# Performance work log

Measured on AMD Instinct MI355X. Metric: run time of the kernel, lower is better.

The kernel has to match this reference:

```python
import jax, jax.numpy as jnp
import numpy as np

B, C, HW = 128, 3, 224
P = 16
D = 256
NH = 8
HD = D // NH
E = 4            # num_experts
K = 2            # top-k
FF = 4 * D
NC = 38
EPS = 1e-5


def _layernorm(x, g, b):
    mu = jnp.mean(x, axis=-1, keepdims=True)
    var = jnp.mean(jnp.square(x - mu), axis=-1, keepdims=True)
    return (x - mu) * jax.lax.rsqrt(var + EPS) * g + b


def setup_inputs() -> dict:
    key = jax.random.key(0)
    ks = jax.random.split(key, 16)
    s = 0.02
    return {
        "x": jax.random.normal(ks[0], (B, C, HW, HW), dtype=jnp.float32),
        "conv_w": jax.random.normal(ks[1], (D, C, P, P), dtype=jnp.float32) * s,
        "conv_b": jnp.zeros((D,), jnp.float32),
        "cls_token": jnp.zeros((1, 1, D), jnp.float32),
        "ln1_g": jnp.ones((D,), jnp.float32),
        "ln1_b": jnp.zeros((D,), jnp.float32),
        "qkv_w": jax.random.normal(ks[2], (3 * D, D), dtype=jnp.float32) * s,
        "qkv_b": jnp.zeros((3 * D,), jnp.float32),
        "out_w": jax.random.normal(ks[3], (D, D), dtype=jnp.float32) * s,
        "out_b": jnp.zeros((D,), jnp.float32),
        "ln2_g": jnp.ones((D,), jnp.float32),
        "ln2_b": jnp.zeros((D,), jnp.float32),
        "router_w": jax.random.normal(ks[4], (E, D), dtype=jnp.float32) * s,
        "router_b": jnp.zeros((E,), jnp.float32),
        "e_w1": jax.random.normal(ks[5], (E, D, FF), dtype=jnp.float32) * s,
        "e_b1": jnp.zeros((E, FF), jnp.float32),
        "e_w2": jax.random.normal(ks[6], (E, FF, D), dtype=jnp.float32) * s,
        "e_b2": jnp.zeros((E, D), jnp.float32),
        "head_w": jax.random.normal(ks[7], (NC, D), dtype=jnp.float32) * s,
        "head_b": jnp.zeros((NC,), jnp.float32),
    }


def reference(x, conv_w, conv_b, cls_token, ln1_g, ln1_b, qkv_w, qkv_b,
              out_w, out_b, ln2_g, ln2_b, router_w, router_b,
              e_w1, e_b1, e_w2, e_b2, head_w, head_b):
    # patch embed: Conv2d(3, D, 16, 16) -> [B, D, 14, 14] -> [B, 196, D]
    h = jax.lax.conv_general_dilated(
        x, conv_w, window_strides=(P, P), padding="VALID",
        dimension_numbers=("NCHW", "OIHW", "NCHW")) + conv_b[None, :, None, None]
    b = h.shape[0]
    tok = h.reshape(b, D, -1).transpose(0, 2, 1)            # [B, 196, D]
    tok = jnp.concatenate([jnp.broadcast_to(cls_token, (b, 1, D)), tok], axis=1)  # [B, 197, D]
    S = tok.shape[1]

    # Multi-head self-attention (pre-norm)
    x2 = _layernorm(tok, ln1_g, ln1_b)
    qkv = x2 @ qkv_w.T + qkv_b                              # [B, S, 3D]
    q, k, v = jnp.split(qkv, 3, axis=-1)
    q = q.reshape(b, S, NH, HD)
    k = k.reshape(b, S, NH, HD)
    v = v.reshape(b, S, NH, HD)
    scores = jnp.einsum("bqhd,bkhd->bhqk", q, k) / np.float32(np.sqrt(HD))
    attn = jax.nn.softmax(scores, axis=-1)
    ao = jnp.einsum("bhqk,bkhd->bqhd", attn, v).reshape(b, S, D)
    ao = ao @ out_w.T + out_b
    tok = tok + ao

    # MoE FFN (pre-norm). NOTE: original code computes top-k routing weights
    # but never multiplies outputs by them — outputs of selected experts are
    # simply summed. We reproduce that faithfully.
    x2 = _layernorm(tok, ln2_g, ln2_b)
    x_flat = x2.reshape(-1, D)                              # [T, D]
    logits = x_flat @ router_w.T + router_b                 # [T, E]
    probs = jax.nn.softmax(logits, axis=-1)
    _topw, topi = jax.lax.top_k(probs, K)                   # topw unused (as in source)
    mask = (topi[..., None] == jnp.arange(E)).any(axis=1)   # [T, E] bool
    out_flat = jnp.zeros_like(x_flat)
    for i in range(E):                                       # fixed small expert count
        hid = jax.nn.gelu(x_flat @ e_w1[i] + e_b1[i], approximate=False)
        out_flat = out_flat + mask[:, i:i + 1].astype(x_flat.dtype) * (hid @ e_w2[i] + e_b2[i])
    tok = tok + out_flat.reshape(b, S, D)

    return tok[:, 0] @ head_w.T + head_b                    # [B, NC]
```

## Files before the change

kernel.cpp:

```cpp
#include <hip/hip_runtime.h>
#include <hip/hip_bf16.h>
#include <math.h>

#define TTOK   25216
#define SEQL   197
#define NBATCH 128
#define DMODEL 256
#define NHEADS 8
#define FFD    1024
#define NEXP   4
#define NCLS   38
#define CONVK  768
#define NPATCH 196
#define CM     25088

typedef unsigned short u16;
typedef unsigned int u32;
using s16x8 = __attribute__((ext_vector_type(8))) short;
using f32x4 = __attribute__((ext_vector_type(4))) float;

__device__ __forceinline__ float b2f(u16 v) {
  union { unsigned u; float f; } x; x.u = (unsigned)v << 16; return x.f;
}
__device__ __forceinline__ u16 f2b(float f) {
  __hip_bfloat16 h = __float2bfloat16(f);
  return *reinterpret_cast<u16*>(&h);
}
__device__ __forceinline__ void gload16(const void* g, void* l) {
  __builtin_amdgcn_global_load_lds(
      (const __attribute__((address_space(1))) void*)g,
      (__attribute__((address_space(3))) void*)l, 16, 0, 0);
}
__device__ __forceinline__ float warp_sum(float v) {
  #pragma unroll
  for (int o = 32; o; o >>= 1) v += __shfl_xor(v, o);
  return v;
}
__device__ __forceinline__ float warp_max(float v) {
  #pragma unroll
  for (int o = 32; o; o >>= 1) v = fmaxf(v, __shfl_xor(v, o));
  return v;
}
__device__ __forceinline__ int fsw(int row) { return (row ^ (row >> 2)) & 3; }

__global__ __launch_bounds__(256) void k_cast2(const float* __restrict__ in,
                                               u16* __restrict__ hi,
                                               u16* __restrict__ lo) {
  int i = (blockIdx.x * 256 + threadIdx.x) * 4;
  float4 v = *(const float4*)&in[i];
  float vv[4] = {v.x, v.y, v.z, v.w};
  u16 h[4], l[4];
  #pragma unroll
  for (int j = 0; j < 4; ++j) {
    h[j] = f2b(vv[j]);
    l[j] = f2b(vv[j] - b2f(h[j]));
  }
  *(uint2*)&hi[i] = *(const uint2*)h;
  *(uint2*)&lo[i] = *(const uint2*)l;
}

__global__ __launch_bounds__(256) void k_conv(const float* __restrict__ x,
                                              const u16* __restrict__ cwh,
                                              const u16* __restrict__ cwl,
                                              const float* __restrict__ cb,
                                              float* __restrict__ tok) {
  const int n0 = blockIdx.x * 128;
  const int m0 = blockIdx.y * 64;
  __shared__ __align__(16) u16 lds[2 * 64 * 40 + 2 * 128 * 32];
  u16* Ah_s = lds;
  u16* Al_s = lds + 64 * 40;
  u16* Wh_s = lds + 2 * 64 * 40;
  u16* Wl_s = lds + 2 * 64 * 40 + 128 * 32;
  const int tid = threadIdx.x;
  const int lane = tid & 63;
  const int wv = tid >> 6;
  const int wr = wv >> 1, wc = wv & 1;
  const int l15 = lane & 15, l4 = lane >> 4;
  f32x4 acc[2][4] = {};

  const int kpos = (tid & 7) * 4;
  long abase[2]; int aldso[2];
  #pragma unroll
  for (int it = 0; it < 2; ++it) {
    int row = it * 32 + (tid >> 3);
    int m = m0 + row;
    int b = m / NPATCH, p = m - b * NPATCH;
    int py = p / 14, px = p - py * 14;
    abase[it] = (long)(b * 3) * 50176 + (py * 16) * 224 + px * 16;
    aldso[it] = row * 80 + kpos * 2;
  }
  long woff[2]; int wofs[2];
  #pragma unroll
  for (int r = 0; r < 2; ++r) {
    int off = r * 4096 + tid * 16;
    int row = off >> 6;
    int c16 = (off >> 4) & 3;
    int kk = (c16 ^ fsw(row)) << 3;
    woff[r] = (long)(n0 + row) * CONVK + kk;
    wofs[r] = off;
  }
  for (int kc = 0; kc < CONVK; kc += 32) {
    #pragma unroll
    for (int r = 0; r < 2; ++r) {
      gload16(cwh + woff[r] + kc, (char*)Wh_s + wofs[r]);
      gload16(cwl + woff[r] + kc, (char*)Wl_s + wofs[r]);
    }
    int k = kc + kpos;
    int c = k >> 8, r8 = k & 255;
    long soff = (long)c * 50176 + (r8 >> 4) * 224 + (r8 & 15);
    #pragma unroll
    for (int it = 0; it < 2; ++it) {
      float4 v = *(const float4*)&x[abase[it] + soff];
      float vv[4] = {v.x, v.y, v.z, v.w};
      u16 h[4], l[4];
      #pragma unroll
      for (int j = 0; j < 4; ++j) {
        h[j] = f2b(vv[j]);
        l[j] = f2b(vv[j] - b2f(h[j]));
      }
      *(uint2*)((char*)Ah_s + aldso[it]) = *(const uint2*)h;
      *(uint2*)((char*)Al_s + aldso[it]) = *(const uint2*)l;
    }
    __syncthreads();
    s16x8 ah[2], al[2], bh[4], bl[4];
    #pragma unroll
    for (int i = 0; i < 2; ++i) {
      int rowa = wr * 32 + i * 16 + l15;
      ah[i] = *(const s16x8*)((const char*)Ah_s + rowa * 80 + l4 * 16);
      al[i] = *(const s16x8*)((const char*)Al_s + rowa * 80 + l4 * 16);
    }
    #pragma unroll
    for (int j = 0; j < 4; ++j) {
      int rowb = wc * 64 + j * 16 + l15;
      int kbb = (l4 ^ fsw(rowb)) << 4;
      bh[j] = *(const s16x8*)((const char*)Wh_s + rowb * 64 + kbb);
      bl[j] = *(const s16x8*)((const char*)Wl_s + rowb * 64 + kbb);
    }
    #pragma unroll
    for (int i = 0; i < 2; ++i)
      #pragma unroll
      for (int j = 0; j < 4; ++j)
        acc[i][j] = __builtin_amdgcn_mfma_f32_16x16x32_bf16(ah[i], bh[j],
                                                            acc[i][j], 0, 0, 0);
    #pragma unroll
    for (int i = 0; i < 2; ++i)
      #pragma unroll
      for (int j = 0; j < 4; ++j)
        acc[i][j] = __builtin_amdgcn_mfma_f32_16x16x32_bf16(ah[i], bl[j],
                                                            acc[i][j], 0, 0, 0);
    #pragma unroll
    for (int i = 0; i < 2; ++i)
      #pragma unroll
      for (int j = 0; j < 4; ++j)
        acc[i][j] = __builtin_amdgcn_mfma_f32_16x16x32_bf16(al[i], bh[j],
                                                            acc[i][j], 0, 0, 0);
    __syncthreads();
  }
  const int mb = m0 + wr * 32 + (l4 << 2);
  const int nb = n0 + wc * 64 + l15;
  #pragma unroll
  for (int i = 0; i < 2; ++i) {
    #pragma unroll
    for (int jf = 0; jf < 4; ++jf) {
      #pragma unroll
      for (int j = 0; j < 4; ++j) {
        int m = mb + i * 16 + j;
        int n = nb + jf * 16;
        int bq = m / NPATCH;
        long cr = (long)bq * SEQL + (m - bq * NPATCH) + 1;
        tok[cr * DMODEL + n] = acc[i][jf][j] + cb[n];
      }
    }
  }
}

__global__ __launch_bounds__(256) void k_lnstat(const float* __restrict__ in,
                                                float2* __restrict__ st) {
  const int row = blockIdx.x * 4 + (threadIdx.x >> 6);
  const int lane = threadIdx.x & 63;
  float4 v = *(const float4*)&in[(size_t)row * DMODEL + lane * 4];
  float s1 = v.x + v.y + v.z + v.w;
  float s2 = v.x * v.x + v.y * v.y + v.z * v.z + v.w * v.w;
  s1 = warp_sum(s1);
  s2 = warp_sum(s2);
  if (lane == 0) {
    float mu = s1 * (1.f / DMODEL);
    float var = s2 * (1.f / DMODEL) - mu * mu;
    st[row] = make_float2(mu, rsqrtf(var + 1e-5f));
  }
}

__global__ __launch_bounds__(256) void k_qkv(const float* __restrict__ tok,
                                             const float2* __restrict__ stats,
                                             const float* __restrict__ g,
                                             const float* __restrict__ bb,
                                             const u16* __restrict__ Wh,
                                             const u16* __restrict__ Wl,
                                             const float* __restrict__ bias,
                                             float* __restrict__ Cf) {
  const int n0 = blockIdx.x * 128;
  const int m0 = blockIdx.y * 128;
  __shared__ __align__(16) u16 lds[2 * 128 * 40 + 2 * 128 * 32];
  u16* Ah_s = lds;
  u16* Al_s = lds + 128 * 40;
  u16* Wh_s = lds + 2 * 128 * 40;
  u16* Wl_s = lds + 2 * 128 * 40 + 128 * 32;
  const int tid = threadIdx.x;
  const int lane = tid & 63;
  const int wv = tid >> 6;
  const int wr = wv >> 1, wc = wv & 1;
  const int l15 = lane & 15, l4 = lane >> 4;
  f32x4 acc[4][4] = {};

  const int kpos = (tid & 7) * 4;
  long atok[4]; float2 st[4]; int aldso[4];
  #pragma unroll
  for (int it = 0; it < 4; ++it) {
    int row = it * 32 + (tid >> 3);
    int m = m0 + row;
    atok[it] = (long)m * DMODEL;
    st[it] = stats[m];
    aldso[it] = row * 80 + kpos * 2;
  }
  long woff[2]; int wofs[2];
  #pragma unroll
  for (int r = 0; r < 2; ++r) {
    int off = r * 4096 + tid * 16;
    int row = off >> 6;
    int c16 = (off >> 4) & 3;
    int kk = (c16 ^ fsw(row)) << 3;
    woff[r] = (long)(n0 + row) * DMODEL + kk;
    wofs[r] = off;
  }
  for (int kc = 0; kc < DMODEL; kc += 32) {
    #pragma unroll
    for (int r = 0; r < 2; ++r) {
      gload16(Wh + woff[r] + kc, (char*)Wh_s + wofs[r]);
      gload16(Wl + woff[r] + kc, (char*)Wl_s + wofs[r]);
    }
    float4 g4 = *(const float4*)&g[kc + kpos];
    float4 b4 = *(const float4*)&bb[kc + kpos];
    float gg[4] = {g4.x, g4.y, g4.z, g4.w};
    float bbv[4] = {b4.x, b4.y, b4.z, b4.w};
    #pragma unroll
    for (int it = 0; it < 4; ++it) {
      float4 v = *(const float4*)&tok[atok[it] + kc + kpos];
      float vv[4] = {v.x, v.y, v.z, v.w};
      u16 h[4], l[4];
      #pragma unroll
      for (int j = 0; j < 4; ++j) {
        float xd = (vv[j] - st[it].x) * st[it].y * gg[j] + bbv[j];
        h[j] = f2b(xd);
        l[j] = f2b(xd - b2f(h[j]));
      }
      *(uint2*)((char*)Ah_s + aldso[it]) = *(const uint2*)h;
      *(uint2*)((char*)Al_s + aldso[it]) = *(const uint2*)l;
    }
    __syncthreads();
    s16x8 ah[4], al[4], bh[4], bl[4];
    #pragma unroll
    for (int i = 0; i < 4; ++i) {
      int rowa = wr * 64 + i * 16 + l15;
      ah[i] = *(const s16x8*)((const char*)Ah_s + rowa * 80 + l4 * 16);
      al[i] = *(const s16x8*)((const char*)Al_s + rowa * 80 + l4 * 16);
      int rowb = wc * 64 + i * 16 + l15;
      int kbb = (l4 ^ fsw(rowb)) << 4;
      bh[i] = *(const s16x8*)((const char*)Wh_s + rowb * 64 + kbb);
      bl[i] = *(const s16x8*)((const char*)Wl_s + rowb * 64 + kbb);
    }
    #pragma unroll
    for (int i = 0; i < 4; ++i)
      #pragma unroll
      for (int j = 0; j < 4; ++j)
        acc[i][j] = __builtin_amdgcn_mfma_f32_16x16x32_bf16(ah[i], bh[j],
                                                            acc[i][j], 0, 0, 0);
    #pragma unroll
    for (int i = 0; i < 4; ++i)
      #pragma unroll
      for (int j = 0; j < 4; ++j)
        acc[i][j] = __builtin_amdgcn_mfma_f32_16x16x32_bf16(ah[i], bl[j],
                                                            acc[i][j], 0, 0, 0);
    #pragma unroll
    for (int i = 0; i < 4; ++i)
      #pragma unroll
      for (int j = 0; j < 4; ++j)
        acc[i][j] = __builtin_amdgcn_mfma_f32_16x16x32_bf16(al[i], bh[j],
                                                            acc[i][j], 0, 0, 0);
    __syncthreads();
  }
  const int mb = m0 + wr * 64 + (l4 << 2);
  const int nb = n0 + wc * 64 + l15;
  #pragma unroll
  for (int i = 0; i < 4; ++i) {
    #pragma unroll
    for (int jf = 0; jf < 4; ++jf) {
      #pragma unroll
      for (int j = 0; j < 4; ++j) {
        int m = mb + i * 16 + j;
        int n = nb + jf * 16;
        Cf[(long)m * 512 + n] = acc[i][jf][j] + bias[n];
      }
    }
  }
}

__global__ void k_cls(const float* __restrict__ cls, float* __restrict__ tok) {
  tok[(size_t)blockIdx.x * SEQL * DMODEL + threadIdx.x] = cls[threadIdx.x];
}

__global__ __launch_bounds__(256) void k_qcls(const float* __restrict__ tok,
                                              const float2* __restrict__ stats,
                                              const float* __restrict__ g,
                                              const float* __restrict__ bb,
                                              const u16* __restrict__ qwh,
                                              const u16* __restrict__ qwl,
                                              const float* __restrict__ qb,
                                              u16* __restrict__ qch,
                                              u16* __restrict__ qcl) {
  const int b = blockIdx.x, n = threadIdx.x;
  __shared__ float xs[DMODEL];
  float2 st = stats[b * SEQL];
  float v = tok[(size_t)b * SEQL * DMODEL + n];
  xs[n] = (v - st.x) * st.y * g[n] + bb[n];
  __syncthreads();
  float val = qb[n];
  #pragma unroll 4
  for (int i = 0; i < 32; ++i) {
    s16x8 wh = *(const s16x8*)(qwh + (size_t)n * DMODEL + i * 8);
    s16x8 wl = *(const s16x8*)(qwl + (size_t)n * DMODEL + i * 8);
    #pragma unroll
    for (int j = 0; j < 8; ++j)
      val = fmaf(b2f((u16)wh[j]) + b2f((u16)wl[j]), xs[i * 8 + j], val);
  }
  u16 h = f2b(val);
  qch[b * DMODEL + n] = h;
  qcl[b * DMODEL + n] = f2b(val - b2f(h));
}

__global__ __launch_bounds__(256) void k_attn_cls(const u16* __restrict__ qch,
                                                  const u16* __restrict__ qcl,
                                                  const float* __restrict__ kvf,
                                                  float* __restrict__ ao) {
  const int w = threadIdx.x >> 6, lane = threadIdx.x & 63;
  const int unit = blockIdx.x * 4 + w;
  const int b = unit >> 3, h = unit & 7;
  __shared__ float Ss[4][200];
  float q[32];
  #pragma unroll
  for (int i = 0; i < 4; ++i) {
    s16x8 vh = *(const s16x8*)(qch + b * DMODEL + h * 32 + i * 8);
    s16x8 vl = *(const s16x8*)(qcl + b * DMODEL + h * 32 + i * 8);
    #pragma unroll
    for (int j = 0; j < 8; ++j) q[i * 8 + j] = b2f((u16)vh[j]) + b2f((u16)vl[j]);
  }
  float sc[4];
  float mx = -1e30f;
  #pragma unroll
  for (int r = 0; r < 4; ++r) {
    int k = lane + 64 * r;
    float s = -1e30f;
    if (k < SEQL) {
      const float* kr = kvf + ((size_t)(b * SEQL + k)) * 512 + h * 32;
      s = 0.f;
      #pragma unroll
      for (int i = 0; i < 8; ++i) {
        float4 kv4 = *(const float4*)(kr + i * 4);
        s = fmaf(kv4.x, q[i * 4 + 0], s);
        s = fmaf(kv4.y, q[i * 4 + 1], s);
        s = fmaf(kv4.z, q[i * 4 + 2], s);
        s = fmaf(kv4.w, q[i * 4 + 3], s);
      }
      s *= 0.17677669529663687f;
    }
    sc[r] = s;
    mx = fmaxf(mx, s);
  }
  mx = warp_max(mx);
  float sm = 0.f;
  #pragma unroll
  for (int r = 0; r < 4; ++r) {
    int k = lane + 64 * r;
    float e = (k < SEQL) ? __expf(sc[r] - mx) : 0.f;
    sc[r] = e;
    sm += e;
  }
  sm = warp_sum(sm);
  float inv = 1.f / sm;
  #pragma unroll
  for (int r = 0; r < 4; ++r) {
    int k = lane + 64 * r;
    if (k < SEQL) Ss[w][k] = sc[r] * inv;
  }
  int d = lane & 31, half = lane >> 5;
  float acc = 0.f;
  for (int i = 0; i < 99; ++i) {
    int k = half * 99 + i;
    if (k < SEQL)
      acc = fmaf(Ss[w][k], kvf[((size_t)(b * SEQL + k)) * 512 + 256 + h * 32 + d], acc);
  }
  acc += __shfl_xor(acc, 32);
  if (lane < 32) ao[(b * NHEADS + h) * 32 + d] = acc;
}

__global__ __launch_bounds__(256) void k_oproj_route(
    const float* __restrict__ ao, const float* __restrict__ ow,
    const float* __restrict__ ob, const float* __restrict__ tok,
    const float* __restrict__ g, const float* __restrict__ bb,
    const float* __restrict__ rw, const float* __restrict__ rb,
    float* __restrict__ tokc, float* __restrict__ x2cf,
    float* __restrict__ maskf) {
  const int b = blockIdx.x, n = threadIdx.x;
  const int w = n >> 6, lane = n & 63;
  __shared__ float xs[DMODEL];
  __shared__ float xd_s[DMODEL];
  __shared__ float red[8];
  __shared__ float lg[4];
  xs[n] = ao[b * DMODEL + n];
  __syncthreads();
  float val = ob[n];
  #pragma unroll 4
  for (int i = 0; i < 64; ++i) {
    float4 wv = *(const float4*)(ow + (size_t)n * DMODEL + i * 4);
    val = fmaf(wv.x, xs[i * 4 + 0], val);
    val = fmaf(wv.y, xs[i * 4 + 1], val);
    val = fmaf(wv.z, xs[i * 4 + 2], val);
    val = fmaf(wv.w, xs[i * 4 + 3], val);
  }
  float t = tok[(size_t)b * SEQL * DMODEL + n] + val;
  tokc[b * DMODEL + n] = t;
  float s1 = warp_sum(t), s2 = warp_sum(t * t);
  if (lane == 0) { red[w] = s1; red[4 + w] = s2; }
  __syncthreads();
  s1 = red[0] + red[1] + red[2] + red[3];
  s2 = red[4] + red[5] + red[6] + red[7];
  float mu = s1 * (1.f / DMODEL);
  float var = s2 * (1.f / DMODEL) - mu * mu;
  float rs = rsqrtf(var + 1e-5f);
  float xd = (t - mu) * rs * g[n] + bb[n];
  x2cf[b * DMODEL + n] = xd;
  xd_s[n] = xd;
  __syncthreads();
  float s = 0.f;
  #pragma unroll
  for (int i = 0; i < 4; ++i) s = fmaf(xd_s[lane + i * 64], rw[w * DMODEL + lane + i * 64], s);
  s = warp_sum(s) + rb[w];
  if (lane == 0) lg[w] = s;
  __syncthreads();
  if (n < NEXP) {
    int e = n;
    int rank = 0;
    #pragma unroll
    for (int j = 0; j < NEXP; ++j)
      if (j != e && (lg[j] > lg[e] || (lg[j] == lg[e] && j < e))) ++rank;
    maskf[b * NEXP + e] = (rank < 2) ? 1.f : 0.f;
  }
}

__global__ __launch_bounds__(256) void k_moe1(const float* __restrict__ x2cf,
                                              const float* __restrict__ w1,
                                              const float* __restrict__ b1,
                                              const float* __restrict__ maskf,
                                              float* __restrict__ hid) {
  const int e = blockIdx.x, t = blockIdx.y;
  if (maskf[t * NEXP + e] == 0.f) return;
  __shared__ float xs[DMODEL];
  const int tid = threadIdx.x;
  xs[tid] = x2cf[t * DMODEL + tid];
  __syncthreads();
  const float* w1e = w1 + (size_t)e * DMODEL * FFD + tid;
  float a0 = 0.f, a1 = 0.f, a2 = 0.f, a3 = 0.f;
  #pragma unroll 4
  for (int k = 0; k < DMODEL; ++k) {
    float xv = xs[k];
    const float* wr_ = w1e + (size_t)k * FFD;
    a0 = fmaf(xv, wr_[0], a0);
    a1 = fmaf(xv, wr_[256], a1);
    a2 = fmaf(xv, wr_[512], a2);
    a3 = fmaf(xv, wr_[768], a3);
  }
  float accs[4] = {a0, a1, a2, a3};
  float* hrow = hid + ((size_t)e * NBATCH + t) * FFD;
  #pragma unroll
  for (int j = 0; j < 4; ++j) {
    float v = accs[j] + b1[e * FFD + tid + j * 256];
    hrow[tid + j * 256] = 0.5f * v * (1.0f + erff(v * 0.70710678118654752f));
  }
}

__global__ __launch_bounds__(256) void k_moe2(const float* __restrict__ hid,
                                              const float* __restrict__ w2,
                                              const float* __restrict__ b2,
                                              const float* __restrict__ maskf,
                                              float* __restrict__ tokc) {
  const int t = blockIdx.x, dc = blockIdx.y;
  const int tid = threadIdx.x;
  const int dl = tid & 127, kh = tid >> 7;
  const int dout = dc * 128 + dl;
  int e0 = 0;
  while (e0 < 3 && maskf[t * NEXP + e0] == 0.f) ++e0;
  int e1 = e0 + 1;
  while (e1 < 3 && maskf[t * NEXP + e1] == 0.f) ++e1;
  __shared__ float hs0[FFD], hs1[FFD];
  const float* h0 = hid + ((size_t)e0 * NBATCH + t) * FFD;
  const float* h1 = hid + ((size_t)e1 * NBATCH + t) * FFD;
  for (int i = tid * 4; i < FFD; i += 1024) {
    *(float4*)&hs0[i] = *(const float4*)&h0[i];
    *(float4*)&hs1[i] = *(const float4*)&h1[i];
  }
  __syncthreads();
  const float* w20 = w2 + (size_t)e0 * FFD * DMODEL + dout;
  const float* w21 = w2 + (size_t)e1 * FFD * DMODEL + dout;
  float a0 = 0.f, a1 = 0.f;
  const int k0 = kh * 512;
  #pragma unroll 8
  for (int k = k0; k < k0 + 512; ++k) {
    a0 = fmaf(hs0[k], w20[(size_t)k * DMODEL], a0);
    a1 = fmaf(hs1[k], w21[(size_t)k * DMODEL], a1);
  }
  __shared__ float red[256];
  red[tid] = a0 + a1;
  __syncthreads();
  if (kh == 0) {
    float full = red[dl] + red[128 + dl] +
                 b2[e0 * DMODEL + dout] + b2[e1 * DMODEL + dout];
    tokc[t * DMODEL + dout] += full;
  }
}

__global__ __launch_bounds__(256) void k_head(const float* __restrict__ tokc,
                                              const float* __restrict__ hw,
                                              const float* __restrict__ hb,
                                              float* __restrict__ out) {
  int b = blockIdx.x;
  int w = threadIdx.x >> 6, lane = threadIdx.x & 63;
  const float* row = tokc + (size_t)b * DMODEL;
  for (int c = w; c < NCLS; c += 4) {
    float s = 0.f;
    for (int d = lane; d < DMODEL; d += 64) s = fmaf(row[d], hw[c * DMODEL + d], s);
    s = warp_sum(s);
    if (lane == 0) out[b * NCLS + c] = s + hb[c];
  }
}

extern "C" void kernel_launch(void* const* d_in, const int* in_sizes, int n_in,
                              void* d_out, int out_size, void* d_ws, size_t ws_size,
                              hipStream_t stream) {
  const float* x      = (const float*)d_in[0];
  const float* conv_w = (const float*)d_in[1];
  const float* conv_b = (const float*)d_in[2];
  const float* cls    = (const float*)d_in[3];
  const float* ln1g   = (const float*)d_in[4];
  const float* ln1b   = (const float*)d_in[5];
  const float* qkv_w  = (const float*)d_in[6];
  const float* qkv_b  = (const float*)d_in[7];
  const float* out_w  = (const float*)d_in[8];
  const float* out_b  = (const float*)d_in[9];
  const float* ln2g   = (const float*)d_in[10];
  const float* ln2b   = (const float*)d_in[11];
  const float* rw     = (const float*)d_in[12];
  const float* rb     = (const float*)d_in[13];
  const float* e_w1   = (const float*)d_in[14];
  const float* e_b1   = (const float*)d_in[15];
  const float* e_w2   = (const float*)d_in[16];
  const float* e_b2   = (const float*)d_in[17];
  const float* head_w = (const float*)d_in[18];
  const float* head_b = (const float*)d_in[19];
  float* out = (float*)d_out;

  char* ws = (char*)d_ws;
  size_t off = 0;
  auto alloc = [&](size_t bytes) {
    void* p = ws + off;
    off += (bytes + 255) & ~(size_t)255;
    return p;
  };
  float*  tok   = (float*)alloc((size_t)TTOK * DMODEL * 4);
  float*  qkvf  = (float*)alloc((size_t)TTOK * 512 * 4);
  float2* stats = (float2*)alloc((size_t)TTOK * 8);
  u16*    cwh   = (u16*)alloc((size_t)DMODEL * CONVK * 2);
  u16*    cwl   = (u16*)alloc((size_t)DMODEL * CONVK * 2);
  u16*    qwh   = (u16*)alloc((size_t)768 * DMODEL * 2);
  u16*    qwl   = (u16*)alloc((size_t)768 * DMODEL * 2);
  u16*    qch   = (u16*)alloc((size_t)NBATCH * DMODEL * 2);
  u16*    qcl   = (u16*)alloc((size_t)NBATCH * DMODEL * 2);
  float*  aocf  = (float*)alloc((size_t)NBATCH * DMODEL * 4);
  float*  tokc  = (float*)alloc((size_t)NBATCH * DMODEL * 4);
  float*  x2cf  = (float*)alloc((size_t)NBATCH * DMODEL * 4);
  float*  maskf = (float*)alloc((size_t)NBATCH * NEXP * 4);
  float*  hid   = (float*)alloc((size_t)NEXP * NBATCH * FFD * 4);

  k_cast2<<<192, 256, 0, stream>>>(conv_w, cwh, cwl);
  k_cast2<<<192, 256, 0, stream>>>(qkv_w, qwh, qwl);

  k_conv<<<dim3(2, CM / 64), 256, 0, stream>>>(x, cwh, cwl, conv_b, tok);
  k_cls<<<NBATCH, DMODEL, 0, stream>>>(cls, tok);

  k_lnstat<<<TTOK / 4, 256, 0, stream>>>(tok, stats);

  k_qkv<<<dim3(4, TTOK / 128), 256, 0, stream>>>(
      tok, stats, ln1g, ln1b, qwh + 256 * DMODEL, qwl + 256 * DMODEL,
      qkv_b + 256, qkvf);

  k_qcls<<<NBATCH, 256, 0, stream>>>(tok, stats, ln1g, ln1b, qwh, qwl, qkv_b,
                                     qch, qcl);

  k_attn_cls<<<NBATCH * NHEADS / 4, 256, 0, stream>>>(qch, qcl, qkvf, aocf);

  k_oproj_route<<<NBATCH, 256, 0, stream>>>(aocf, out_w, out_b, tok,
                                            ln2g, ln2b, rw, rb,
                                            tokc, x2cf, maskf);

  k_moe1<<<dim3(NEXP, NBATCH), 256, 0, stream>>>(x2cf, e_w1, e_b1, maskf, hid);
  k_moe2<<<dim3(NBATCH, 2), 256, 0, stream>>>(hid, e_w2, e_b2, maskf, tokc);

  k_head<<<NBATCH, 256, 0, stream>>>(tokc, head_w, head_b, out);
}
```

Measured before the change: 212.9 us.

## Double-buffer weights and prefetch activations in conv and QKV GEMMs, enlarge conv tile

The conv and QKV GEMM kernels now double-buffer the weight tiles in LDS and prefetch the next K-chunk of activations into registers while the current chunk's MFMAs run, so global loads overlap with compute. The conv tile grows from 64 to 128 rows per block, giving more reuse per weight load and fewer blocks. The A-tile LDS row stride shrinks from 80 to 72 bytes, which requires split 8-byte reads, to change the bank pattern. The trade-off is higher register and LDS use per block, which may lower occupancy.

```diff
diff --git a/kernel.cpp b/kernel.cpp
--- a/kernel.cpp
+++ b/kernel.cpp
@@ -16,6 +16,7 @@
 
 typedef unsigned short u16;
 typedef unsigned int u32;
+using s16x4 = __attribute__((ext_vector_type(4))) short;
 using s16x8 = __attribute__((ext_vector_type(8))) short;
 using f32x4 = __attribute__((ext_vector_type(4))) float;
 
@@ -42,6 +43,12 @@
   return v;
 }
 __device__ __forceinline__ int fsw(int row) { return (row ^ (row >> 2)) & 3; }
+__device__ __forceinline__ s16x8 ldA72(const u16* base, int rowa, int l4) {
+  const char* p = (const char*)base + rowa * 72 + l4 * 16;
+  s16x4 a = *(const s16x4*)p;
+  s16x4 b = *(const s16x4*)(p + 8);
+  return __builtin_shufflevector(a, b, 0, 1, 2, 3, 4, 5, 6, 7);
+}
 
 __global__ __launch_bounds__(256) void k_cast2(const float* __restrict__ in,
                                                u16* __restrict__ hi,
@@ -65,29 +72,28 @@
                                               const float* __restrict__ cb,
                                               float* __restrict__ tok) {
   const int n0 = blockIdx.x * 128;
-  const int m0 = blockIdx.y * 64;
-  __shared__ __align__(16) u16 lds[2 * 64 * 40 + 2 * 128 * 32];
+  const int m0 = blockIdx.y * 128;
+  __shared__ __align__(16) u16 lds[25600];
   u16* Ah_s = lds;
-  u16* Al_s = lds + 64 * 40;
-  u16* Wh_s = lds + 2 * 64 * 40;
-  u16* Wl_s = lds + 2 * 64 * 40 + 128 * 32;
+  u16* Al_s = lds + 4608;
+  u16* Wbuf = lds + 9216;
   const int tid = threadIdx.x;
   const int lane = tid & 63;
   const int wv = tid >> 6;
   const int wr = wv >> 1, wc = wv & 1;
   const int l15 = lane & 15, l4 = lane >> 4;
-  f32x4 acc[2][4] = {};
+  f32x4 acc[4][4] = {};
 
   const int kpos = (tid & 7) * 4;
-  long abase[2]; int aldso[2];
-  #pragma unroll
-  for (int it = 0; it < 2; ++it) {
+  long abase[4]; int aldso[4];
+  #pragma unroll
+  for (int it = 0; it < 4; ++it) {
     int row = it * 32 + (tid >> 3);
     int m = m0 + row;
     int b = m / NPATCH, p = m - b * NPATCH;
     int py = p / 14, px = p - py * 14;
     abase[it] = (long)(b * 3) * 50176 + (py * 16) * 224 + px * 16;
-    aldso[it] = row * 80 + kpos * 2;
+    aldso[it] = row * 72 + kpos * 2;
   }
   long woff[2]; int wofs[2];
   #pragma unroll
@@ -99,19 +105,23 @@
     woff[r] = (long)(n0 + row) * CONVK + kk;
     wofs[r] = off;
   }
+  #pragma unroll
+  for (int r = 0; r < 2; ++r) {
+    gload16(cwh + woff[r], (char*)Wbuf + wofs[r]);
+    gload16(cwl + woff[r], (char*)Wbuf + 8192 + wofs[r]);
+  }
+  float4 xr[4];
+  {
+    int c = kpos >> 8, r8 = kpos & 255;
+    long soff = (long)c * 50176 + (r8 >> 4) * 224 + (r8 & 15);
+    #pragma unroll
+    for (int it = 0; it < 4; ++it) xr[it] = *(const float4*)&x[abase[it] + soff];
+  }
+  int cur = 0;
   for (int kc = 0; kc < CONVK; kc += 32) {
     #pragma unroll
-    for (int r = 0; r < 2; ++r) {
-      gload16(cwh + woff[r] + kc, (char*)Wh_s + wofs[r]);
-      gload16(cwl + woff[r] + kc, (char*)Wl_s + wofs[r]);
-    }
-    int k = kc + kpos;
-    int c = k >> 8, r8 = k & 255;
-    long soff = (long)c * 50176 + (r8 >> 4) * 224 + (r8 & 15);
-    #pragma unroll
-    for (int it = 0; it < 2; ++it) {
-      float4 v = *(const float4*)&x[abase[it] + soff];
-      float vv[4] = {v.x, v.y, v.z, v.w};
+    for (int it = 0; it < 4; ++it) {
+      float vv[4] = {xr[it].x, xr[it].y, xr[it].z, xr[it].w};
       u16 h[4], l[4];
       #pragma unroll
       for (int j = 0; j < 4; ++j) {
@@ -122,44 +132,56 @@
       *(uint2*)((char*)Al_s + aldso[it]) = *(const uint2*)l;
     }
     __syncthreads();
-    s16x8 ah[2], al[2], bh[4], bl[4];
-    #pragma unroll
-    for (int i = 0; i < 2; ++i) {
-      int rowa = wr * 32 + i * 16 + l15;
-      ah[i] = *(const s16x8*)((const char*)Ah_s + rowa * 80 + l4 * 16);
-      al[i] = *(const s16x8*)((const char*)Al_s + rowa * 80 + l4 * 16);
-    }
-    #pragma unroll
-    for (int j = 0; j < 4; ++j) {
-      int rowb = wc * 64 + j * 16 + l15;
+    if (kc + 32 < CONVK) {
+      char* wdst = (char*)Wbuf + ((cur ^ 1) << 14);
+      #pragma unroll
+      for (int r = 0; r < 2; ++r) {
+        gload16(cwh + woff[r] + kc + 32, wdst + wofs[r]);
+        gload16(cwl + woff[r] + kc + 32, wdst + 8192 + wofs[r]);
+      }
+      int k = kc + 32 + kpos;
+      int c = k >> 8, r8 = k & 255;
+      long soff = (long)c * 50176 + (r8 >> 4) * 224 + (r8 & 15);
+      #pragma unroll
+      for (int it = 0; it < 4; ++it) xr[it] = *(const float4*)&x[abase[it] + soff];
+    }
+    const char* Wcur = (const char*)Wbuf + (cur << 14);
+    s16x8 ah[4], al[4], bh[4], bl[4];
+    #pragma unroll
+    for (int i = 0; i < 4; ++i) {
+      int rowa = wr * 64 + i * 16 + l15;
+      ah[i] = ldA72(Ah_s, rowa, l4);
+      al[i] = ldA72(Al_s, rowa, l4);
+      int rowb = wc * 64 + i * 16 + l15;
       int kbb = (l4 ^ fsw(rowb)) << 4;
-      bh[j] = *(const s16x8*)((const char*)Wh_s + rowb * 64 + kbb);
-      bl[j] = *(const s16x8*)((const char*)Wl_s + rowb * 64 + kbb);
-    }
-    #pragma unroll
-    for (int i = 0; i < 2; ++i)
+      bh[i] = *(const s16x8*)(Wcur + rowb * 64 + kbb);
+      bl[i] = *(const s16x8*)(Wcur + 8192 + rowb * 64 + kbb);
+    }
+    #pragma unroll
+    for (int i = 0; i < 4; ++i)
       #pragma unroll
       for (int j = 0; j < 4; ++j)
         acc[i][j] = __builtin_amdgcn_mfma_f32_16x16x32_bf16(ah[i], bh[j],
                                                             acc[i][j], 0, 0, 0);
     #pragma unroll
-    for (int i = 0; i < 2; ++i)
+    for (int i = 0; i < 4; ++i)
       #pragma unroll
       for (int j = 0; j < 4; ++j)
         acc[i][j] = __builtin_amdgcn_mfma_f32_16x16x32_bf16(ah[i], bl[j],
                                                             acc[i][j], 0, 0, 0);
     #pragma unroll
-    for (int i = 0; i < 2; ++i)
+    for (int i = 0; i < 4; ++i)
       #pragma unroll
       for (int j = 0; j < 4; ++j)
         acc[i][j] = __builtin_amdgcn_mfma_f32_16x16x32_bf16(al[i], bh[j],
                                                             acc[i][j], 0, 0, 0);
     __syncthreads();
-  }
-  const int mb = m0 + wr * 32 + (l4 << 2);
+    cur ^= 1;
+  }
+  const int mb = m0 + wr * 64 + (l4 << 2);
   const int nb = n0 + wc * 64 + l15;
   #pragma unroll
-  for (int i = 0; i < 2; ++i) {
+  for (int i = 0; i < 4; ++i) {
     #pragma unroll
     for (int jf = 0; jf < 4; ++jf) {
       #pragma unroll
@@ -200,11 +222,10 @@
                                              float* __restrict__ Cf) {
   const int n0 = blockIdx.x * 128;
   const int m0 = blockIdx.y * 128;
-  __shared__ __align__(16) u16 lds[2 * 128 * 40 + 2 * 128 * 32];
+  __shared__ __align__(16) u16 lds[25600];
   u16* Ah_s = lds;
-  u16* Al_s = lds + 128 * 40;
-  u16* Wh_s = lds + 2 * 128 * 40;
-  u16* Wl_s = lds + 2 * 128 * 40 + 128 * 32;
+  u16* Al_s = lds + 4608;
+  u16* Wbuf = lds + 9216;
   const int tid = threadIdx.x;
   const int lane = tid & 63;
   const int wv = tid >> 6;
@@ -220,7 +241,7 @@
     int m = m0 + row;
     atok[it] = (long)m * DMODEL;
     st[it] = stats[m];
-    aldso[it] = row * 80 + kpos * 2;
+    aldso[it] = row * 72 + kpos * 2;
   }
   long woff[2]; int wofs[2];
   #pragma unroll
@@ -232,20 +253,23 @@
     woff[r] = (long)(n0 + row) * DMODEL + kk;
     wofs[r] = off;
   }
+  #pragma unroll
+  for (int r = 0; r < 2; ++r) {
+    gload16(Wh + woff[r], (char*)Wbuf + wofs[r]);
+    gload16(Wl + woff[r], (char*)Wbuf + 8192 + wofs[r]);
+  }
+  float4 xr[4], gr, br;
+  #pragma unroll
+  for (int it = 0; it < 4; ++it) xr[it] = *(const float4*)&tok[atok[it] + kpos];
+  gr = *(const float4*)&g[kpos];
+  br = *(const float4*)&bb[kpos];
+  int cur = 0;
   for (int kc = 0; kc < DMODEL; kc += 32) {
-    #pragma unroll
-    for (int r = 0; r < 2; ++r) {
-      gload16(Wh + woff[r] + kc, (char*)Wh_s + wofs[r]);
-      gload16(Wl + woff[r] + kc, (char*)Wl_s + wofs[r]);
-    }
-    float4 g4 = *(const float4*)&g[kc + kpos];
-    float4 b4 = *(const float4*)&bb[kc + kpos];
-    float gg[4] = {g4.x, g4.y, g4.z, g4.w};
-    float bbv[4] = {b4.x, b4.y, b4.z, b4.w};
+    float gg[4] = {gr.x, gr.y, gr.z, gr.w};
+    float bbv[4] = {br.x, br.y, br.z, br.w};
     #pragma unroll
     for (int it = 0; it < 4; ++it) {
-      float4 v = *(const float4*)&tok[atok[it] + kc + kpos];
-      float vv[4] = {v.x, v.y, v.z, v.w};
+      float vv[4] = {xr[it].x, xr[it].y, xr[it].z, xr[it].w};
       u16 h[4], l[4];
       #pragma unroll
       for (int j = 0; j < 4; ++j) {
@@ -257,16 +281,30 @@
       *(uint2*)((char*)Al_s + aldso[it]) = *(const uint2*)l;
     }
     __syncthreads();
+    if (kc + 32 < DMODEL) {
+      char* wdst = (char*)Wbuf + ((cur ^ 1) << 14);
+      #pragma unroll
+      for (int r = 0; r < 2; ++r) {
+        gload16(Wh + woff[r] + kc + 32, wdst + wofs[r]);
+        gload16(Wl + woff[r] + kc + 32, wdst + 8192 + wofs[r]);
+      }
+      #pragma unroll
+      for (int it = 0; it < 4; ++it)
+        xr[it] = *(const float4*)&tok[atok[it] + kc + 32 + kpos];
+      gr = *(const float4*)&g[kc + 32 + kpos];
+      br = *(const float4*)&bb[kc + 32 + kpos];
+    }
+    const char* Wcur = (const char*)Wbuf + (cur << 14);
     s16x8 ah[4], al[4], bh[4], bl[4];
     #pragma unroll
     for (int i = 0; i < 4; ++i) {
       int rowa = wr * 64 + i * 16 + l15;
-      ah[i] = *(const s16x8*)((const char*)Ah_s + rowa * 80 + l4 * 16);
-      al[i] = *(const s16x8*)((const char*)Al_s + rowa * 80 + l4 * 16);
+      ah[i] = ldA72(Ah_s, rowa, l4);
+      al[i] = ldA72(Al_s, rowa, l4);
       int rowb = wc * 64 + i * 16 + l15;
       int kbb = (l4 ^ fsw(rowb)) << 4;
-      bh[i] = *(const s16x8*)((const char*)Wh_s + rowb * 64 + kbb);
-      bl[i] = *(const s16x8*)((const char*)Wl_s + rowb * 64 + kbb);
+      bh[i] = *(const s16x8*)(Wcur + rowb * 64 + kbb);
+      bl[i] = *(const s16x8*)(Wcur + 8192 + rowb * 64 + kbb);
     }
     #pragma unroll
     for (int i = 0; i < 4; ++i)
@@ -287,6 +325,7 @@
         acc[i][j] = __builtin_amdgcn_mfma_f32_16x16x32_bf16(al[i], bh[j],
                                                             acc[i][j], 0, 0, 0);
     __syncthreads();
+    cur ^= 1;
   }
   const int mb = m0 + wr * 64 + (l4 << 2);
   const int nb = n0 + wc * 64 + l15;
@@ -592,7 +631,7 @@
   k_cast2<<<192, 256, 0, stream>>>(conv_w, cwh, cwl);
   k_cast2<<<192, 256, 0, stream>>>(qkv_w, qwh, qwl);
 
-  k_conv<<<dim3(2, CM / 64), 256, 0, stream>>>(x, cwh, cwl, conv_b, tok);
+  k_conv<<<dim3(2, CM / 128), 256, 0, stream>>>(x, cwh, cwl, conv_b, tok);
   k_cls<<<NBATCH, DMODEL, 0, stream>>>(cls, tok);
 
   k_lnstat<<<TTOK / 4, 256, 0, stream>>>(tok, stats);
```

Result: no change. 211.3 us (-0.8%).
